# Kernel optimization log

Hardware: AMD Instinct MI355X
Metric: run time of the kernel (lower is better)

Reference implementation:

```python
import jax, jax.numpy as jnp
import numpy as np

B, C, M, T = 2, 512, 16, 128
H = 8
D = C // H  # 64, divisible by 4 for 2D RoPE
G = C // 4  # GroupNorm groups = 128
S = M * T


def group_norm(x, scale, bias, groups=G, eps=1e-5):
    b, c, m, t = x.shape
    xg = x.reshape(b, groups, c // groups, m, t)
    mu = xg.mean(axis=(2, 3, 4), keepdims=True)
    var = xg.var(axis=(2, 3, 4), keepdims=True)
    xn = ((xg - mu) * jax.lax.rsqrt(var + eps)).reshape(b, c, m, t)
    return xn * scale[None, :, None, None] + bias[None, :, None, None]


def dwsep_conv(x, dw, pw):
    # depthwise 3x3 (groups=C) then pointwise 1x1
    y = jax.lax.conv_general_dilated(
        x, dw, window_strides=(1, 1), padding='SAME',
        dimension_numbers=('NCHW', 'HWIO', 'NCHW'), feature_group_count=x.shape[1])
    return jnp.einsum('bcmt,cd->bdmt', y, pw)


def rope2d(x):
    # x: [B,H,M,T,D]; first D/2 dims rotated by freq index m, last D/2 by time index t
    d = x.shape[-1]
    dh = d // 2
    q = dh // 2
    inv = 1.0 / (10000.0 ** (jnp.arange(q, dtype=jnp.float32) / q))

    def rot(v, ang):
        h = v.shape[-1] // 2
        v1, v2 = v[..., :h], v[..., h:]
        c, s = jnp.cos(ang), jnp.sin(ang)
        return jnp.concatenate([v1 * c - v2 * s, v1 * s + v2 * c], axis=-1)

    ang_f = jnp.arange(x.shape[2], dtype=jnp.float32)[:, None] * inv  # [M,q]
    ang_t = jnp.arange(x.shape[3], dtype=jnp.float32)[:, None] * inv  # [T,q]
    xf = rot(x[..., :dh], ang_f[:, None, :])  # broadcast over T
    xt = rot(x[..., dh:], ang_t)
    return jnp.concatenate([xf, xt], axis=-1)


def setup_inputs() -> dict:
    key = jax.random.key(0)
    ks = jax.random.split(key, 14)
    s = 0.02
    return {
        'x': jax.random.normal(ks[0], (B, C, M, T), jnp.float32),
        'lengths': jax.random.randint(ks[1], (B,), T // 2, T + 1),
        'gn_scale': jnp.ones((C,), jnp.float32),
        'gn_bias': jnp.zeros((C,), jnp.float32),
        'dw_q': jax.random.normal(ks[2], (3, 3, 1, C), jnp.float32) * s,
        'dw_k': jax.random.normal(ks[3], (3, 3, 1, C), jnp.float32) * s,
        'dw_v': jax.random.normal(ks[4], (3, 3, 1, C), jnp.float32) * s,
        'pw_q': jax.random.normal(ks[5], (C, C), jnp.float32) * s,
        'pw_k': jax.random.normal(ks[6], (C, C), jnp.float32) * s,
        'pw_v': jax.random.normal(ks[7], (C, C), jnp.float32) * s,
        'attn_w': jax.random.normal(ks[8], (C, C), jnp.float32) * s,
        'attn_b': jnp.zeros((C,), jnp.float32),
        'out_w': jax.random.normal(ks[9], (C, C), jnp.float32) * s,
        'out_b': jnp.zeros((C,), jnp.float32),
    }


def reference(x, lengths, gn_scale, gn_bias, dw_q, dw_k, dw_v, pw_q, pw_k, pw_v,
              attn_w, attn_b, out_w, out_b):
    residual = x
    xn = group_norm(x, gn_scale, gn_bias)

    def to_heads(y):  # [B,C,M,T] -> [B,H,M,T,D]
        return y.reshape(B, H, D, M, T).transpose(0, 1, 3, 4, 2)

    q = rope2d(to_heads(dwsep_conv(xn, dw_q, pw_q)))
    k = rope2d(to_heads(dwsep_conv(xn, dw_k, pw_k)))
    v = to_heads(dwsep_conv(xn, dw_v, pw_v))

    q = q.reshape(B, H, S, D)
    k = k.reshape(B, H, S, D)
    v = v.reshape(B, H, S, D)

    scores = jnp.einsum('bhsd,bhkd->bhsk', q, k) / np.sqrt(D).astype(np.float32)
    valid_t = jnp.arange(T)[None, :] < lengths[:, None]        # [B,T]
    valid = jnp.tile(valid_t, (1, M))                          # [B,S], token idx = m*T + t
    scores = jnp.where(valid[:, None, None, :], scores, jnp.float32(-1e9))
    attn = jax.nn.softmax(scores, axis=-1)
    o = jnp.einsum('bhsk,bhkd->bhsd', attn, v)                 # [B,H,S,D]

    o = o.transpose(0, 2, 1, 3).reshape(B, S, C)
    o = o @ attn_w + attn_b                                    # block output proj
    o = o.reshape(B, M, T, C).transpose(0, 3, 1, 2)            # [B,C,M,T]
    out = jnp.einsum('bcmt,cd->bdmt', o, out_w) + out_b[None, :, None, None]
    return residual + out
```

## Files before the change

kernel.cpp:

```cpp
#include <hip/hip_runtime.h>
#include <math.h>

#define CCH 512
#define SSQ 2048
#define MTOT 4096

typedef __bf16 bf16;
typedef __bf16 bf16x8 __attribute__((ext_vector_type(8)));
typedef __bf16 bf16x4 __attribute__((ext_vector_type(4)));
typedef float  f32x4  __attribute__((ext_vector_type(4)));

__global__ void gn_stats_kernel(const float* __restrict__ x,
                                float* __restrict__ mu, float* __restrict__ rstd) {
    __shared__ float s_sum[256], s_sq[256];
    int bg = blockIdx.x;
    long base = (long)bg * 8192;
    int tid = threadIdx.x;
    float sum = 0.f, sq = 0.f;
#pragma unroll
    for (int r = 0; r < 32; ++r) {
        float v = x[base + r*256 + tid];
        sum += v; sq += v*v;
    }
    s_sum[tid] = sum; s_sq[tid] = sq;
    __syncthreads();
    for (int off = 128; off > 0; off >>= 1) {
        if (tid < off) { s_sum[tid] += s_sum[tid+off]; s_sq[tid] += s_sq[tid+off]; }
        __syncthreads();
    }
    if (tid == 0) {
        float m = s_sum[0] * (1.f/8192.f);
        float v = s_sq[0]  * (1.f/8192.f) - m*m;
        mu[bg] = m;
        rstd[bg] = rsqrtf(v + 1e-5f);
    }
}

__global__ void wconv_kernel(const float* __restrict__ w0, const float* __restrict__ w1,
                             const float* __restrict__ w2, const float* __restrict__ w3,
                             const float* __restrict__ w4, bf16* __restrict__ out) {
    __shared__ float t[64][65];
    const float* srcs[5] = {w0, w1, w2, w3, w4};
    const float* W = srcs[blockIdx.z];
    bf16* D = out + (long)blockIdx.z * (CCH*CCH);
    int k0 = blockIdx.x*64, n0 = blockIdx.y*64;
    int tid = threadIdx.x;
    int cI = tid & 63, r4 = tid >> 6;
#pragma unroll
    for (int p = 0; p < 16; ++p) {
        int kr = p*4 + r4;
        t[kr][cI] = W[(long)(k0+kr)*CCH + n0 + cI];
    }
    __syncthreads();
#pragma unroll
    for (int p = 0; p < 16; ++p) {
        int nr = p*4 + r4;
        D[(long)(n0+nr)*CCH + k0 + cI] = (bf16)t[cI][nr];
    }
}

__global__ void tn_kernel(const float* __restrict__ x, const float* __restrict__ mu,
                          const float* __restrict__ rstd, const float* __restrict__ gsc,
                          const float* __restrict__ gbs, bf16* __restrict__ xnT) {
    __shared__ float t[64][65];
    int s0 = blockIdx.x*64, c0 = blockIdx.y*64, b = blockIdx.z;
    int tid = threadIdx.x;
    int cI = tid & 63, r4 = tid >> 6;
#pragma unroll
    for (int p = 0; p < 16; ++p) {
        int cr = p*4 + r4;
        t[cr][cI] = x[((long)(b*CCH + c0 + cr))*SSQ + s0 + cI];
    }
    __syncthreads();
#pragma unroll
    for (int p = 0; p < 16; ++p) {
        int sr = p*4 + r4;
        int c = c0 + cI;
        int g = b*128 + (c >> 2);
        float v = (t[cI][sr] - mu[g]) * rstd[g] * gsc[c] + gbs[c];
        xnT[((long)(b*SSQ + s0 + sr))*CCH + c] = (bf16)v;
    }
}

__global__ __launch_bounds__(256) void dw3_kernel(const bf16* __restrict__ xnT,
        const float* __restrict__ dwq, const float* __restrict__ dwk,
        const float* __restrict__ dwv,
        bf16* __restrict__ yq, bf16* __restrict__ yk, bf16* __restrict__ yv) {
    int tid = threadIdx.x;
    int cc = (tid & 63) * 8;
    int s  = blockIdx.x*4 + (tid >> 6);
    int sl = s & (SSQ-1);
    int b  = s >> 11;
    int m = sl >> 7, t = sl & 127;
    float aq[8] = {}, ak[8] = {}, av[8] = {};
#pragma unroll
    for (int di = 0; di < 3; ++di) {
        int m2 = m + di - 1;
        if ((unsigned)m2 >= 16u) continue;
#pragma unroll
        for (int dj = 0; dj < 3; ++dj) {
            int t2 = t + dj - 1;
            if ((unsigned)t2 >= 128u) continue;
            bf16x8 xv = *(const bf16x8*)(xnT + ((long)(b*SSQ + m2*128 + t2))*CCH + cc);
            int wi = (di*3 + dj)*CCH + cc;
#pragma unroll
            for (int i = 0; i < 8; ++i) {
                float xf = (float)xv[i];
                aq[i] += xf * dwq[wi+i];
                ak[i] += xf * dwk[wi+i];
                av[i] += xf * dwv[wi+i];
            }
        }
    }
    bf16x8 oq, ok, ov;
#pragma unroll
    for (int i = 0; i < 8; ++i) { oq[i] = (bf16)aq[i]; ok[i] = (bf16)ak[i]; ov[i] = (bf16)av[i]; }
    long o = (long)s*CCH + cc;
    *(bf16x8*)(yq + o) = oq;
    *(bf16x8*)(yk + o) = ok;
    *(bf16x8*)(yv + o) = ov;
}

template<int MODE>
__global__ __launch_bounds__(256) void gemm_bf16(const bf16* __restrict__ A,
        const bf16* __restrict__ Wt, const float* __restrict__ bias,
        const float* __restrict__ resid, void* __restrict__ outv) {
    __shared__ bf16 As[64*32];
    __shared__ bf16 Bs[64*32];
    int m0 = blockIdx.x*64, n0 = blockIdx.y*64;
    int tid = threadIdx.x, lane = tid & 63, wid = tid >> 6;
    int sw = wid & 1, nw = wid >> 1;
    int col = lane & 15, quad = lane >> 4;
    f32x4 acc[2][2] = {};
    int srow = tid >> 2, koff = (tid & 3)*8;
    const bf16* Ag = A  + (long)(m0 + srow)*CCH + koff;
    const bf16* Bg = Wt + (long)(n0 + srow)*CCH + koff;
    bf16* Asp = As + srow*32 + koff;
    bf16* Bsp = Bs + srow*32 + koff;
    const bf16* Ab = As + (sw*32 + col)*32 + quad*8;
    const bf16* Bb = Bs + (nw*32 + col)*32 + quad*8;
    for (int k0 = 0; k0 < CCH; k0 += 32) {
        bf16x8 a = *(const bf16x8*)(Ag + k0);
        bf16x8 w = *(const bf16x8*)(Bg + k0);
        __syncthreads();
        *(bf16x8*)Asp = a;
        *(bf16x8*)Bsp = w;
        __syncthreads();
        bf16x8 af0 = *(const bf16x8*)(Ab);
        bf16x8 af1 = *(const bf16x8*)(Ab + 16*32);
        bf16x8 wf0 = *(const bf16x8*)(Bb);
        bf16x8 wf1 = *(const bf16x8*)(Bb + 16*32);
        acc[0][0] = __builtin_amdgcn_mfma_f32_16x16x32_bf16(af0, wf0, acc[0][0], 0,0,0);
        acc[0][1] = __builtin_amdgcn_mfma_f32_16x16x32_bf16(af0, wf1, acc[0][1], 0,0,0);
        acc[1][0] = __builtin_amdgcn_mfma_f32_16x16x32_bf16(af1, wf0, acc[1][0], 0,0,0);
        acc[1][1] = __builtin_amdgcn_mfma_f32_16x16x32_bf16(af1, wf1, acc[1][1], 0,0,0);
    }
    int nb = n0 + nw*32;
    int mb = m0 + sw*32;
    if (MODE == 0 || MODE == 1) {
        bf16* outp = (bf16*)outv;
        float invf = __expf(-(float)col * 0.5756462732485114f);
        bool tHalf = (nb & 32) != 0;
        const float sc = (MODE == 0) ? 0.125f : 1.0f;
#pragma unroll
        for (int st = 0; st < 2; ++st)
#pragma unroll
            for (int r = 0; r < 4; ++r) {
                int row = mb + st*16 + quad*4 + r;
                int sl = row & (SSQ-1);
                float pos = tHalf ? (float)(sl & 127) : (float)(sl >> 7);
                float ang = pos * invf;
                float sn, cs;
                __sincosf(ang, &sn, &cs);
                float x1 = acc[st][0][r], x2 = acc[st][1][r];
                outp[(long)row*CCH + nb + col]      = (bf16)((x1*cs - x2*sn)*sc);
                outp[(long)row*CCH + nb + 16 + col] = (bf16)((x1*sn + x2*cs)*sc);
            }
    } else if (MODE == 2) {
        bf16* outp = (bf16*)outv;
#pragma unroll
        for (int st = 0; st < 2; ++st)
#pragma unroll
            for (int nt = 0; nt < 2; ++nt) {
                int n = nb + nt*16 + col;
                int row0 = mb + st*16 + quad*4;
                int b = row0 >> 11, sl0 = row0 & (SSQ-1);
                bf16x4 pk;
#pragma unroll
                for (int r = 0; r < 4; ++r) pk[r] = (bf16)acc[st][nt][r];
                *(bf16x4*)(outp + ((long)(b*CCH + n))*SSQ + sl0) = pk;
            }
    } else if (MODE == 3) {
        bf16* outp = (bf16*)outv;
#pragma unroll
        for (int nt = 0; nt < 2; ++nt) {
            int n = nb + nt*16 + col;
            float bv = bias[n];
#pragma unroll
            for (int st = 0; st < 2; ++st)
#pragma unroll
                for (int r = 0; r < 4; ++r)
                    outp[(long)(mb + st*16 + quad*4 + r)*CCH + n] = (bf16)(acc[st][nt][r] + bv);
        }
    } else {
        float* outp = (float*)outv;
#pragma unroll
        for (int st = 0; st < 2; ++st)
#pragma unroll
            for (int nt = 0; nt < 2; ++nt) {
                int n = nb + nt*16 + col;
                float bv = bias[n];
                int row0 = mb + st*16 + quad*4;
                int b = row0 >> 11, sl0 = row0 & (SSQ-1);
                long off = ((long)(b*CCH + n))*SSQ + sl0;
                float4 rr = *(const float4*)(resid + off);
                float4 o4;
                o4.x = acc[st][nt][0] + bv + rr.x;
                o4.y = acc[st][nt][1] + bv + rr.y;
                o4.z = acc[st][nt][2] + bv + rr.z;
                o4.w = acc[st][nt][3] + bv + rr.w;
                *(float4*)(outp + off) = o4;
            }
    }
}

__global__ __launch_bounds__(256) void attn_kernel(
        const bf16* __restrict__ qb, const bf16* __restrict__ kb,
        const bf16* __restrict__ vb, const int* __restrict__ lengths,
        bf16* __restrict__ o) {
    __shared__ bf16 KVs[2][2*64*80];
    __shared__ bf16 Ps[4][16*72];
    int b = blockIdx.z, h = blockIdx.y;
    int tid = threadIdx.x, wid = tid >> 6, lane = tid & 63;
    int col = lane & 15, quad = lane >> 4;
    int q0 = blockIdx.x*64 + wid*16;
    int lenb = lengths[b];

    const char* sp[5];
    long sstr[5];
#pragma unroll
    for (int i = 0; i < 5; ++i) {
        int off = i*4096 + tid*16;
        if (off < 10240) {
            int row = off / 160, rb = off % 160;
            sp[i] = (const char*)kb + ((long)(b*SSQ + row))*1024 + h*128 + rb;
            sstr[i] = 1024;
        } else {
            int o2 = off - 10240;
            int d = o2 / 160, rb = o2 % 160;
            sp[i] = (const char*)vb + ((long)(b*CCH + h*64 + d))*4096 + rb;
            sstr[i] = 2;
        }
    }

    const bf16* qp = qb + (long)(b*SSQ)*CCH + h*64;
    bf16x8 qf[2];
#pragma unroll
    for (int dc = 0; dc < 2; ++dc)
        qf[dc] = *(const bf16x8*)(qp + (long)(q0 + col)*CCH + dc*32 + quad*8);

    f32x4 of[4] = {};
    float lsum = 0.f;
    bf16* pw = Ps[wid];

    bf16x8 sreg[5];
#pragma unroll
    for (int i = 0; i < 5; ++i) sreg[i] = *(const bf16x8*)(sp[i]);
#pragma unroll
    for (int i = 0; i < 5; ++i)
        *(bf16x8*)((char*)&KVs[0][0] + i*4096 + tid*16) = sreg[i];
    __syncthreads();

    for (int t = 0; t < 32; ++t) {
        int kt = t*64;
        const bf16* K = KVs[t & 1];
        const bf16* V = KVs[t & 1] + 64*80;
        if (t < 31) {
#pragma unroll
            for (int i = 0; i < 5; ++i)
                sreg[i] = *(const bf16x8*)(sp[i] + (long)(kt + 64)*sstr[i]);
        }
        f32x4 acc[4] = {};
#pragma unroll
        for (int sub = 0; sub < 4; ++sub)
#pragma unroll
            for (int dc = 0; dc < 2; ++dc) {
                bf16x8 kf = *(const bf16x8*)(K + (sub*16 + col)*80 + dc*32 + quad*8);
                acc[sub] = __builtin_amdgcn_mfma_f32_16x16x32_bf16(kf, qf[dc], acc[sub], 0,0,0);
            }
#pragma unroll
        for (int sub = 0; sub < 4; ++sub) {
            bf16x4 pk;
#pragma unroll
            for (int r = 0; r < 4; ++r) {
                int key = kt + sub*16 + quad*4 + r;
                float p = ((key & 127) < lenb) ? __expf(acc[sub][r]) : 0.f;
                lsum += p;
                pk[r] = (bf16)p;
            }
            *(bf16x4*)(pw + col*72 + sub*16 + quad*4) = pk;
        }
#pragma unroll
        for (int ks = 0; ks < 2; ++ks) {
            bf16x8 pf = *(const bf16x8*)(pw + col*72 + ks*32 + quad*8);
#pragma unroll
            for (int dt = 0; dt < 4; ++dt) {
                bf16x8 vf = *(const bf16x8*)(V + (dt*16 + col)*80 + ks*32 + quad*8);
                of[dt] = __builtin_amdgcn_mfma_f32_16x16x32_bf16(pf, vf, of[dt], 0,0,0);
            }
        }
        if (t < 31) {
            char* nb2 = (char*)&KVs[(t + 1) & 1][0];
#pragma unroll
            for (int i = 0; i < 5; ++i)
                *(bf16x8*)(nb2 + i*4096 + tid*16) = sreg[i];
        }
        __syncthreads();
    }
    lsum += __shfl_xor(lsum, 16);
    lsum += __shfl_xor(lsum, 32);
    float invl = 1.f / lsum;
    float ir[4];
#pragma unroll
    for (int r = 0; r < 4; ++r) ir[r] = __shfl(invl, quad*4 + r);
    bf16* ob = o + (long)(b*SSQ + q0)*CCH + h*64;
#pragma unroll
    for (int dt = 0; dt < 4; ++dt)
#pragma unroll
        for (int r = 0; r < 4; ++r)
            ob[(long)(quad*4 + r)*CCH + dt*16 + col] = (bf16)(of[dt][r] * ir[r]);
}

extern "C" void kernel_launch(void* const* d_in, const int* in_sizes, int n_in,
                              void* d_out, int out_size, void* d_ws, size_t ws_size,
                              hipStream_t stream) {
    const float* x        = (const float*)d_in[0];
    const int*   lengths  = (const int*)  d_in[1];
    const float* gn_scale = (const float*)d_in[2];
    const float* gn_bias  = (const float*)d_in[3];
    const float* dw_q     = (const float*)d_in[4];
    const float* dw_k     = (const float*)d_in[5];
    const float* dw_v     = (const float*)d_in[6];
    const float* pw_q     = (const float*)d_in[7];
    const float* pw_k     = (const float*)d_in[8];
    const float* pw_v     = (const float*)d_in[9];
    const float* attn_w   = (const float*)d_in[10];
    const float* attn_b   = (const float*)d_in[11];
    const float* out_w    = (const float*)d_in[12];
    const float* out_b    = (const float*)d_in[13];
    float* out = (float*)d_out;

    char* w = (char*)d_ws;
    float* mu   = (float*)w;
    float* rstd = (float*)(w + 1024);
    bf16* wT    = (bf16*)(w + 4096);
    bf16* wTq = wT;
    bf16* wTk = wT + 1*CCH*CCH;
    bf16* wTv = wT + 2*CCH*CCH;
    bf16* wTa = wT + 3*CCH*CCH;
    bf16* wTo = wT + 4*CCH*CCH;
    bf16* xnT  = (bf16*)(w + 0x00300000);
    bf16* yqT  = (bf16*)(w + 0x00700000);
    bf16* ykT  = (bf16*)(w + 0x00B00000);
    bf16* yvT  = (bf16*)(w + 0x00F00000);
    bf16* qbf  = (bf16*)(w + 0x01300000);
    bf16* kbf  = (bf16*)(w + 0x01700000);
    bf16* vbf  = (bf16*)(w + 0x01B00000);
    bf16* obf  = (bf16*)(w + 0x01F00000);
    bf16* tmpb = (bf16*)(w + 0x02300000);

    gn_stats_kernel<<<256, 256, 0, stream>>>(x, mu, rstd);
    wconv_kernel<<<dim3(8,8,5), 256, 0, stream>>>(pw_q, pw_k, pw_v, attn_w, out_w, wT);
    tn_kernel<<<dim3(32,8,2), 256, 0, stream>>>(x, mu, rstd, gn_scale, gn_bias, xnT);
    dw3_kernel<<<MTOT/4, 256, 0, stream>>>(xnT, dw_q, dw_k, dw_v, yqT, ykT, yvT);

    dim3 gg(MTOT/64, CCH/64);
    gemm_bf16<0><<<gg, 256, 0, stream>>>(yqT, wTq, nullptr, nullptr, qbf);
    gemm_bf16<1><<<gg, 256, 0, stream>>>(ykT, wTk, nullptr, nullptr, kbf);
    gemm_bf16<2><<<gg, 256, 0, stream>>>(yvT, wTv, nullptr, nullptr, vbf);

    attn_kernel<<<dim3(SSQ/64, 8, 2), 256, 0, stream>>>(qbf, kbf, vbf, lengths, obf);

    gemm_bf16<3><<<gg, 256, 0, stream>>>(obf, wTa, attn_b, nullptr, tmpb);
    gemm_bf16<4><<<gg, 256, 0, stream>>>(tmpb, wTo, out_b, x, out);
}
```

Measured before the change: 187.7 us.

## Use direct global-to-LDS loads with XOR swizzle in GEMM and repad attention KV tiles

The projection GEMM now stages 64-wide K tiles straight from global memory into LDS with global_load_lds, so the data no longer passes through registers, and applies an XOR swizzle to avoid bank conflicts. Each iteration now issues twice as many MFMAs between barriers. The attention kernel drops the old 80-element rows, which loaded padding bytes, and loads exactly 64 elements per K/V row into LDS rows padded to 88 elements, using 4 loads per thread instead of 5. In exchange, the GEMM still has no double buffering, and the global_load_lds path depends on the layout that one wave writes matching the swizzled reads.

After: 179.8 us. 4.2% less time.

```diff
diff --git a/kernel.cpp b/kernel.cpp
--- a/kernel.cpp
+++ b/kernel.cpp
@@ -9,6 +9,12 @@
 typedef __bf16 bf16x8 __attribute__((ext_vector_type(8)));
 typedef __bf16 bf16x4 __attribute__((ext_vector_type(4)));
 typedef float  f32x4  __attribute__((ext_vector_type(4)));
+
+#define AS1 __attribute__((address_space(1)))
+#define AS3 __attribute__((address_space(3)))
+__device__ __forceinline__ void glds16(const void* g, void* l) {
+    __builtin_amdgcn_global_load_lds((const AS1 void*)g, (AS3 void*)l, 16, 0, 0);
+}
 
 __global__ void gn_stats_kernel(const float* __restrict__ x,
                                 float* __restrict__ mu, float* __restrict__ rstd) {
@@ -125,35 +131,63 @@
 __global__ __launch_bounds__(256) void gemm_bf16(const bf16* __restrict__ A,
         const bf16* __restrict__ Wt, const float* __restrict__ bias,
         const float* __restrict__ resid, void* __restrict__ outv) {
-    __shared__ bf16 As[64*32];
-    __shared__ bf16 Bs[64*32];
+    __shared__ bf16 As[64*64];
+    __shared__ bf16 Bs[64*64];
     int m0 = blockIdx.x*64, n0 = blockIdx.y*64;
     int tid = threadIdx.x, lane = tid & 63, wid = tid >> 6;
     int sw = wid & 1, nw = wid >> 1;
     int col = lane & 15, quad = lane >> 4;
     f32x4 acc[2][2] = {};
-    int srow = tid >> 2, koff = (tid & 3)*8;
-    const bf16* Ag = A  + (long)(m0 + srow)*CCH + koff;
-    const bf16* Bg = Wt + (long)(n0 + srow)*CCH + koff;
-    bf16* Asp = As + srow*32 + koff;
-    bf16* Bsp = Bs + srow*32 + koff;
-    const bf16* Ab = As + (sw*32 + col)*32 + quad*8;
-    const bf16* Bb = Bs + (nw*32 + col)*32 + quad*8;
-    for (int k0 = 0; k0 < CCH; k0 += 32) {
-        bf16x8 a = *(const bf16x8*)(Ag + k0);
-        bf16x8 w = *(const bf16x8*)(Bg + k0);
+
+    const char* gA[2]; const char* gB[2];
+    char* ldsA[2]; char* ldsB[2];
+#pragma unroll
+    for (int p = 0; p < 2; ++p) {
+        int ci = wid*64 + lane + p*256;
+        int row = ci >> 3;
+        int c = (ci & 7) ^ (row & 7);
+        gA[p] = (const char*)A  + ((long)(m0+row)*CCH + c*8)*2;
+        gB[p] = (const char*)Wt + ((long)(n0+row)*CCH + c*8)*2;
+        ldsA[p] = (char*)As + wid*1024 + p*4096;
+        ldsB[p] = (char*)Bs + wid*1024 + p*4096;
+    }
+    int rowA = sw*32 + col, rowB = nw*32 + col;
+
+    for (int k0 = 0; k0 < CCH; k0 += 64) {
         __syncthreads();
-        *(bf16x8*)Asp = a;
-        *(bf16x8*)Bsp = w;
+#pragma unroll
+        for (int p = 0; p < 2; ++p) {
+            glds16(gA[p] + k0*2, ldsA[p]);
+            glds16(gB[p] + k0*2, ldsB[p]);
+        }
         __syncthreads();
-        bf16x8 af0 = *(const bf16x8*)(Ab);
-        bf16x8 af1 = *(const bf16x8*)(Ab + 16*32);
-        bf16x8 wf0 = *(const bf16x8*)(Bb);
-        bf16x8 wf1 = *(const bf16x8*)(Bb + 16*32);
-        acc[0][0] = __builtin_amdgcn_mfma_f32_16x16x32_bf16(af0, wf0, acc[0][0], 0,0,0);
-        acc[0][1] = __builtin_amdgcn_mfma_f32_16x16x32_bf16(af0, wf1, acc[0][1], 0,0,0);
-        acc[1][0] = __builtin_amdgcn_mfma_f32_16x16x32_bf16(af1, wf0, acc[1][0], 0,0,0);
-        acc[1][1] = __builtin_amdgcn_mfma_f32_16x16x32_bf16(af1, wf1, acc[1][1], 0,0,0);
+        bf16x8 af[2][2], bf[2][2];
+#pragma unroll
+        for (int mt = 0; mt < 2; ++mt) {
+            int r = rowA + mt*16;
+#pragma unroll
+            for (int ks = 0; ks < 2; ++ks) {
+                int c = (ks*4 + quad) ^ (r & 7);
+                af[mt][ks] = *(const bf16x8*)((char*)As + r*128 + c*16);
+            }
+        }
+#pragma unroll
+        for (int nt = 0; nt < 2; ++nt) {
+            int r = rowB + nt*16;
+#pragma unroll
+            for (int ks = 0; ks < 2; ++ks) {
+                int c = (ks*4 + quad) ^ (r & 7);
+                bf[nt][ks] = *(const bf16x8*)((char*)Bs + r*128 + c*16);
+            }
+        }
+#pragma unroll
+        for (int ks = 0; ks < 2; ++ks)
+#pragma unroll
+            for (int mt = 0; mt < 2; ++mt)
+#pragma unroll
+                for (int nt = 0; nt < 2; ++nt)
+                    acc[mt][nt] = __builtin_amdgcn_mfma_f32_16x16x32_bf16(
+                        af[mt][ks], bf[nt][ks], acc[mt][nt], 0,0,0);
     }
     int nb = n0 + nw*32;
     int mb = m0 + sw*32;
@@ -224,11 +258,13 @@
     }
 }
 
+#define KVROW 88
+#define KVIMG (64*KVROW*2)
 __global__ __launch_bounds__(256) void attn_kernel(
         const bf16* __restrict__ qb, const bf16* __restrict__ kb,
         const bf16* __restrict__ vb, const int* __restrict__ lengths,
         bf16* __restrict__ o) {
-    __shared__ bf16 KVs[2][2*64*80];
+    __shared__ char KVs[2][2*KVIMG];
     __shared__ bf16 Ps[4][16*72];
     int b = blockIdx.z, h = blockIdx.y;
     int tid = threadIdx.x, wid = tid >> 6, lane = tid & 63;
@@ -236,21 +272,16 @@
     int q0 = blockIdx.x*64 + wid*16;
     int lenb = lengths[b];
 
-    const char* sp[5];
-    long sstr[5];
-#pragma unroll
-    for (int i = 0; i < 5; ++i) {
-        int off = i*4096 + tid*16;
-        if (off < 10240) {
-            int row = off / 160, rb = off % 160;
-            sp[i] = (const char*)kb + ((long)(b*SSQ + row))*1024 + h*128 + rb;
-            sstr[i] = 1024;
-        } else {
-            int o2 = off - 10240;
-            int d = o2 / 160, rb = o2 % 160;
-            sp[i] = (const char*)vb + ((long)(b*CCH + h*64 + d))*4096 + rb;
-            sstr[i] = 2;
-        }
+    const char* gp[4]; long gstep[4]; int ldsoff[4];
+#pragma unroll
+    for (int p = 0; p < 4; ++p) {
+        int idx = tid + p*256;
+        int isV = idx >> 9;
+        int r = (idx >> 3) & 63;
+        int c = idx & 7;
+        if (!isV) { gp[p] = (const char*)kb + ((long)(b*SSQ + r))*1024 + h*128 + c*16; gstep[p] = 65536; }
+        else      { gp[p] = (const char*)vb + ((long)(b*CCH + h*64 + r))*4096 + c*16;  gstep[p] = 128; }
+        ldsoff[p] = isV*KVIMG + r*176 + c*16;
     }
 
     const bf16* qp = qb + (long)(b*SSQ)*CCH + h*64;
@@ -263,29 +294,28 @@
     float lsum = 0.f;
     bf16* pw = Ps[wid];
 
-    bf16x8 sreg[5];
-#pragma unroll
-    for (int i = 0; i < 5; ++i) sreg[i] = *(const bf16x8*)(sp[i]);
-#pragma unroll
-    for (int i = 0; i < 5; ++i)
-        *(bf16x8*)((char*)&KVs[0][0] + i*4096 + tid*16) = sreg[i];
+    bf16x8 sreg[4];
+#pragma unroll
+    for (int p = 0; p < 4; ++p) sreg[p] = *(const bf16x8*)(gp[p]);
+#pragma unroll
+    for (int p = 0; p < 4; ++p) *(bf16x8*)(KVs[0] + ldsoff[p]) = sreg[p];
     __syncthreads();
 
     for (int t = 0; t < 32; ++t) {
         int kt = t*64;
-        const bf16* K = KVs[t & 1];
-        const bf16* V = KVs[t & 1] + 64*80;
+        const bf16* K = (const bf16*)KVs[t & 1];
+        const bf16* V = (const bf16*)(KVs[t & 1] + KVIMG);
         if (t < 31) {
 #pragma unroll
-            for (int i = 0; i < 5; ++i)
-                sreg[i] = *(const bf16x8*)(sp[i] + (long)(kt + 64)*sstr[i]);
+            for (int p = 0; p < 4; ++p)
+                sreg[p] = *(const bf16x8*)(gp[p] + (long)(t+1)*gstep[p]);
         }
         f32x4 acc[4] = {};
 #pragma unroll
         for (int sub = 0; sub < 4; ++sub)
 #pragma unroll
             for (int dc = 0; dc < 2; ++dc) {
-                bf16x8 kf = *(const bf16x8*)(K + (sub*16 + col)*80 + dc*32 + quad*8);
+                bf16x8 kf = *(const bf16x8*)(K + (sub*16 + col)*KVROW + dc*32 + quad*8);
                 acc[sub] = __builtin_amdgcn_mfma_f32_16x16x32_bf16(kf, qf[dc], acc[sub], 0,0,0);
             }
 #pragma unroll
@@ -305,15 +335,14 @@
             bf16x8 pf = *(const bf16x8*)(pw + col*72 + ks*32 + quad*8);
 #pragma unroll
             for (int dt = 0; dt < 4; ++dt) {
-                bf16x8 vf = *(const bf16x8*)(V + (dt*16 + col)*80 + ks*32 + quad*8);
+                bf16x8 vf = *(const bf16x8*)(V + (dt*16 + col)*KVROW + ks*32 + quad*8);
                 of[dt] = __builtin_amdgcn_mfma_f32_16x16x32_bf16(pf, vf, of[dt], 0,0,0);
             }
         }
         if (t < 31) {
-            char* nb2 = (char*)&KVs[(t + 1) & 1][0];
-#pragma unroll
-            for (int i = 0; i < 5; ++i)
-                *(bf16x8*)(nb2 + i*4096 + tid*16) = sreg[i];
+            char* nb2 = KVs[(t + 1) & 1];
+#pragma unroll
+            for (int p = 0; p < 4; ++p) *(bf16x8*)(nb2 + ldsoff[p]) = sreg[p];
         }
         __syncthreads();
     }
```
